# Performance work log

Measured on AMD Instinct MI355X. Metric: run time of the kernel, lower is better.

## Reference

```python
import jax, jax.numpy as jnp
import numpy as np
from jax import lax

B, D, T = 8, 128, 4096
Q, C = 30, 1024


def setup_inputs() -> dict:
    key = jax.random.key(0)
    k1, k2 = jax.random.split(key)
    x = jax.random.normal(k1, (B, D, T), dtype=jnp.float32)
    codebooks = jax.random.normal(k2, (Q, C, D), dtype=jnp.float32)
    return {"x": x, "codebooks": codebooks}


def _vq_step(residual, cb):
    # residual: [B, T, D], cb: [C, D]
    # argmin over squared euclidean distance; ||r||^2 term is constant per row
    scores = -2.0 * jnp.einsum("btd,cd->btc", residual, cb) + jnp.sum(cb * cb, axis=-1)  # [B,T,C]
    idx = jnp.argmin(scores, axis=-1)          # [B,T]
    quant = cb[idx]                            # [B,T,D] gather
    # commitment loss: mse(quantize.detach(), residual)
    loss = jnp.mean((lax.stop_gradient(quant) - residual) ** 2)
    # straight-through estimator
    quant_st = residual + lax.stop_gradient(quant - residual)
    new_residual = residual - lax.stop_gradient(quant)
    return new_residual, (quant_st, loss)


def reference(x, codebooks):
    # x: [B, D, T] -> [B, T, D]
    xt = jnp.transpose(x, (0, 2, 1))
    _, (quants, losses) = lax.scan(_vq_step, xt, codebooks)  # quants: [Q,B,T,D]
    quantized = jnp.sum(quants, axis=0)                      # [B,T,D]
    quantized = jnp.transpose(quantized, (0, 2, 1))          # [B,D,T]
    commit_loss = jnp.sum(losses)
    return quantized, commit_loss
```

## Files before the change

### kernel.cpp

```cpp
#include <hip/hip_runtime.h>
#include <stdint.h>

#define B_ 8
#define D_ 128
#define T_ 4096
#define Q_ 30
#define C_ 1024

typedef __attribute__((ext_vector_type(8))) _Float16 half8;
typedef __attribute__((ext_vector_type(4))) float float4_;

__device__ __align__(16) _Float16 g_half[(size_t)Q_*8*16384];

typedef __attribute__((address_space(3))) void lds_void;
typedef __attribute__((address_space(1))) const void gbl_void;
__device__ __forceinline__ void gld16(const void* g, void* l){
  __builtin_amdgcn_global_load_lds((gbl_void*)g, (lds_void*)l, 16, 0, 0);
}

__global__ void rvq_prep(const float* __restrict__ cb, float* __restrict__ sumsq){
  int g    = blockIdx.x*128 + (threadIdx.x>>1);
  int half = threadIdx.x & 1;
  const float* src = cb + (size_t)g*D_ + half*64;
  double s = 0.0;
#pragma unroll
  for (int i=0;i<64;i+=4){
    float4_ f = *(const float4_*)(src+i);
    s += (double)f.x*f.x + (double)f.y*f.y + (double)f.z*f.z + (double)f.w*f.w;
  }
  s += __shfl_xor(s, 1);
  if (!half) sumsq[g] = (float)s;
}

__global__ void rvq_split(const float* __restrict__ cb){
  const int bI   = blockIdx.x;
  const int tid  = threadIdx.x;
  const int crel = tid>>1, part = tid&1;
  const int swz  = crel & 15;
  const float* src = cb + ((size_t)bI*128 + crel)*128 + part*64;
  _Float16* dst = g_half + ((size_t)bI<<14) + (crel<<7);
#pragma unroll
  for (int i=0;i<8;++i){
    float4_ f0 = *(const float4_*)(src + i*8);
    float4_ f1 = *(const float4_*)(src + i*8 + 4);
    half8 h;
    h[0]=(_Float16)f0.x; h[1]=(_Float16)f0.y; h[2]=(_Float16)f0.z; h[3]=(_Float16)f0.w;
    h[4]=(_Float16)f1.x; h[5]=(_Float16)f1.y; h[6]=(_Float16)f1.z; h[7]=(_Float16)f1.w;
    const int kg  = part*8 + i;
    const int kgs = kg ^ swz;
    *(half8*)&dst[kgs<<3] = h;
  }
}

__global__ __launch_bounds__(256,1) void rvq_main(
    const float* __restrict__ x, const float* __restrict__ cb,
    const float* __restrict__ sumsq, double* __restrict__ lossAcc,
    float* __restrict__ out)
{
  __shared__ _Float16 sBh[2*16384];
  __shared__ float sCS[4][32][16][2];
  __shared__ int   sCI[4][32][16][2];
  __shared__ int   sI4[4][32][4];
  __shared__ float sCcQ[1024];

  const int tid  = threadIdx.x;
  const int wv   = tid>>6;
  const int ln   = tid&63;
  const int col  = ln&15;
  const int quad = ln>>4;
  const int blk  = blockIdx.x;
  const int b    = blk>>5;
  const int t0   = ((blk&31)<<7) + (wv<<5);

  double rmast[2][4][8];
#pragma unroll
  for (int rt=0;rt<2;++rt){
    const int t = t0 + rt*16 + col;
#pragma unroll
    for (int kc=0;kc<4;++kc)
#pragma unroll
      for (int j=0;j<8;++j){
        const int d = kc*32 + quad*8 + j;
        rmast[rt][kc][j] = (double)x[((size_t)b*D_ + d)*T_ + t];
      }
  }

  half8 ah[2][4];
  auto makeAB = [&](){
#pragma unroll
    for (int rt=0;rt<2;++rt)
#pragma unroll
      for (int kc=0;kc<4;++kc){
        half8 h;
#pragma unroll
        for (int j=0;j<8;++j) h[j] = (_Float16)(float)rmast[rt][kc][j];
        ah[rt][kc] = h;
      }
  };
  makeAB();

  auto stage = [&](int c){
    const char* gsrc = (const char*)g_half + ((size_t)c<<15) + (wv<<13) + (ln<<4);
    char* ldst = (char*)sBh + ((c&1)<<15) + (wv<<13) + (ln<<4);
#pragma unroll
    for (int it=0; it<8; ++it)
      gld16(gsrc + it*1024, ldst + it*1024);
  };

  for (int i=tid; i<1024; i+=256) sCcQ[i] = sumsq[i];
  stage(0);
  __syncthreads();

  double lossd = 0.0;

  for (int q=0;q<Q_;++q){
    const float* cbq = cb + (size_t)q*C_*D_;

    float m1[2][4], m2[2][4]; int i1[2][4], i2[2][4];
#pragma unroll
    for (int rt=0;rt<2;++rt)
#pragma unroll
      for (int rg=0;rg<4;++rg){
        m1[rt][rg]=3.0e38f; i1[rt][rg]=0;
        m2[rt][rg]=3.0e38f; i2[rt][rg]=0;
      }

    for (int ch=0; ch<8; ++ch){
      const int gstep = q*8 + ch;
      const int nxt   = (gstep+1 < Q_*8) ? gstep+1 : 0;
      stage(nxt);
      asm volatile("s_waitcnt vmcnt(8)" ::: "memory");
      asm volatile("s_barrier" ::: "memory");
      const int slot = (gstep&1)<<14;

#pragma unroll
      for (int itc=0; itc<4; ++itc){
        float4_ acc[2][2];
#pragma unroll
        for (int a=0;a<2;++a)
#pragma unroll
          for (int c2=0;c2<2;++c2) acc[a][c2] = (float4_){0.f,0.f,0.f,0.f};
#pragma unroll
        for (int kc=0;kc<4;++kc){
          const int kgs = ((kc<<2) + quad) ^ col;
          half8 bf[2];
#pragma unroll
          for (int ct=0;ct<2;++ct){
            const int n = itc*32 + ct*16 + col;
            bf[ct] = *(const half8*)&sBh[slot + (n<<7) + (kgs<<3)];
          }
#pragma unroll
          for (int rt=0;rt<2;++rt)
#pragma unroll
            for (int ct=0;ct<2;++ct)
              acc[rt][ct] = __builtin_amdgcn_mfma_f32_16x16x32_f16(ah[rt][kc], bf[ct], acc[rt][ct], 0,0,0);
        }
#pragma unroll
        for (int ct=0;ct<2;++ct){
          const float cc = sCcQ[(ch<<7) + itc*32 + ct*16 + col];
          const int cid  = ch*8 + itc*2 + ct;
#pragma unroll
          for (int rt=0;rt<2;++rt)
#pragma unroll
            for (int rg=0;rg<4;++rg){
              float s = fmaf(-2.0f, acc[rt][ct][rg], cc);
              if (s < m1[rt][rg]) {
                m2[rt][rg]=m1[rt][rg]; i2[rt][rg]=i1[rt][rg];
                m1[rt][rg]=s;          i1[rt][rg]=cid;
              } else if (s < m2[rt][rg]) {
                m2[rt][rg]=s;          i2[rt][rg]=cid;
              }
            }
        }
      }
      if (ch != 7)
        asm volatile("s_barrier" ::: "memory");
    }

#pragma unroll
    for (int rt=0;rt<2;++rt)
#pragma unroll
      for (int rg=0;rg<4;++rg){
        const int row = rt*16 + quad*4 + rg;
        sCS[wv][row][col][0] = m1[rt][rg];  sCI[wv][row][col][0] = (i1[rt][rg]<<4)+col;
        sCS[wv][row][col][1] = m2[rt][rg];  sCI[wv][row][col][1] = (i2[rt][rg]<<4)+col;
      }

    if (ln < 32){
      const int row = ln;
      float b0=3.0e38f,b1=3.0e38f,b2=3.0e38f,b3=3.0e38f;
      int   e0=0x7fffffff,e1=0x7fffffff,e2=0x7fffffff,e3=0x7fffffff;
#pragma unroll
      for (int c2=0;c2<32;++c2){
        const float s = sCS[wv][row][c2>>1][c2&1];
        const int  id = sCI[wv][row][c2>>1][c2&1];
        const bool l0 = (s<b0)||(s==b0&&id<e0);
        const bool l1 = (s<b1)||(s==b1&&id<e1);
        const bool l2 = (s<b2)||(s==b2&&id<e2);
        const bool l3 = (s<b3)||(s==b3&&id<e3);
        if (l3){
          b3 = l2 ? b2 : s;  e3 = l2 ? e2 : id;
          if (l2){
            b2 = l1 ? b1 : s;  e2 = l1 ? e1 : id;
            if (l1){
              b1 = l0 ? b0 : s;  e1 = l0 ? e0 : id;
              if (l0){ b0 = s; e0 = id; }
            }
          }
        }
      }
      sI4[wv][row][0]=e0; sI4[wv][row][1]=e1; sI4[wv][row][2]=e2; sI4[wv][row][3]=e3;
    }

#pragma unroll
    for (int rt=0;rt<2;++rt){
      const int m = rt*16 + col;
      double bestS = 1.0e300; int bestJ = 0x7fffffff;
#pragma unroll
      for (int cnd=0;cnd<4;++cnd){
        const int jj = sI4[wv][m][cnd];
        const float* p = cbq + ((size_t)jj<<7) + (quad<<3);
        double s = 0.0;
#pragma unroll
        for (int kc=0;kc<4;++kc){
          float4_ a0 = *(const float4_*)(p + kc*32);
          float4_ a1 = *(const float4_*)(p + kc*32 + 4);
          float fv[8] = {a0.x,a0.y,a0.z,a0.w,a1.x,a1.y,a1.z,a1.w};
#pragma unroll
          for (int j=0;j<8;++j){
            double cd = (double)fv[j];
            s += cd*(cd - 2.0*rmast[rt][kc][j]);
          }
        }
        s += __shfl_xor(s, 16); s += __shfl_xor(s, 32);
        if ((s < bestS) || (s == bestS && jj < bestJ)){ bestS = s; bestJ = jj; }
      }
      const float* pw = cbq + ((size_t)bestJ<<7) + (quad<<3);
#pragma unroll
      for (int kc=0;kc<4;++kc){
        float4_ w0 = *(const float4_*)(pw + kc*32);
        float4_ w1 = *(const float4_*)(pw + kc*32 + 4);
        float fw[8] = {w0.x,w0.y,w0.z,w0.w,w1.x,w1.y,w1.z,w1.w};
#pragma unroll
        for (int j=0;j<8;++j){
          double rn = rmast[rt][kc][j] - (double)fw[j];
          rmast[rt][kc][j] = rn;
          lossd += rn*rn;
        }
      }
    }
    makeAB();
    if (q+1 < Q_){
      for (int i=tid; i<1024; i+=256) sCcQ[i] = sumsq[(q+1)*1024 + i];
    }
    __syncthreads();
  }

#pragma unroll
  for (int rt=0;rt<2;++rt){
    const int t = t0 + rt*16 + col;
#pragma unroll
    for (int kc=0;kc<4;++kc)
#pragma unroll
      for (int j=0;j<8;++j){
        const int d = kc*32 + quad*8 + j;
        const size_t o = ((size_t)b*D_ + d)*T_ + t;
        out[o] = (float)((double)x[o] - rmast[rt][kc][j]);
      }
  }
#pragma unroll
  for (int mk=1; mk<64; mk<<=1) lossd += __shfl_xor(lossd, mk);
  if (ln==0) atomicAdd(lossAcc, lossd);
}

__global__ void rvq_fin(const double* __restrict__ lossAcc, float* __restrict__ out){
  out[(size_t)B_*D_*T_] = (float)(*lossAcc * (1.0/((double)B_*(double)D_*(double)T_)));
}

extern "C" void kernel_launch(void* const* d_in, const int* in_sizes, int n_in,
                              void* d_out, int out_size, void* d_ws, size_t ws_size,
                              hipStream_t stream) {
  const float* x  = (const float*)d_in[0];
  const float* cb = (const float*)d_in[1];
  float* out      = (float*)d_out;
  double* lossAcc = (double*)d_ws;
  float*  sumsq   = (float*)((char*)d_ws + 256);

  hipMemsetAsync(d_ws, 0, 256, stream);
  rvq_prep <<<Q_*C_/128, 256, 0, stream>>>(cb, sumsq);
  rvq_split<<<Q_*8,      256, 0, stream>>>(cb);
  rvq_main <<<(B_*T_)/128, 256, 0, stream>>>(x, cb, sumsq, lossAcc, out);
  rvq_fin  <<<1, 1, 0, stream>>>(lossAcc, out);
}
```

Baseline: 1.944 ms.

## Give each wave a private triple-buffered LDS ring to drop workgroup barriers

```diff
diff --git a/kernel.cpp b/kernel.cpp
--- a/kernel.cpp
+++ b/kernel.cpp
@@ -10,7 +10,7 @@
 typedef __attribute__((ext_vector_type(8))) _Float16 half8;
 typedef __attribute__((ext_vector_type(4))) float float4_;
 
-__device__ __align__(16) _Float16 g_half[(size_t)Q_*8*16384];
+__device__ __align__(16) _Float16 g_half[(size_t)Q_*32*4096];
 
 typedef __attribute__((address_space(3))) void lds_void;
 typedef __attribute__((address_space(1))) const void gbl_void;
@@ -33,20 +33,21 @@
 }
 
 __global__ void rvq_split(const float* __restrict__ cb){
-  const int bI   = blockIdx.x;
+  const int gs   = blockIdx.x;
   const int tid  = threadIdx.x;
-  const int crel = tid>>1, part = tid&1;
+  const int crel = tid>>3;
+  const int part = tid&7;
   const int swz  = crel & 15;
-  const float* src = cb + ((size_t)bI*128 + crel)*128 + part*64;
-  _Float16* dst = g_half + ((size_t)bI<<14) + (crel<<7);
-#pragma unroll
-  for (int i=0;i<8;++i){
+  const float* src = cb + ((size_t)gs*32 + crel)*128 + part*16;
+  _Float16* dst = g_half + ((size_t)gs<<12) + (crel<<7);
+#pragma unroll
+  for (int i=0;i<2;++i){
     float4_ f0 = *(const float4_*)(src + i*8);
     float4_ f1 = *(const float4_*)(src + i*8 + 4);
     half8 h;
     h[0]=(_Float16)f0.x; h[1]=(_Float16)f0.y; h[2]=(_Float16)f0.z; h[3]=(_Float16)f0.w;
     h[4]=(_Float16)f1.x; h[5]=(_Float16)f1.y; h[6]=(_Float16)f1.z; h[7]=(_Float16)f1.w;
-    const int kg  = part*8 + i;
+    const int kg  = part*2 + i;
     const int kgs = kg ^ swz;
     *(half8*)&dst[kgs<<3] = h;
   }
@@ -57,9 +58,9 @@
     const float* __restrict__ sumsq, double* __restrict__ lossAcc,
     float* __restrict__ out)
 {
-  __shared__ _Float16 sBh[2*16384];
-  __shared__ float sCS[4][32][16][2];
-  __shared__ int   sCI[4][32][16][2];
+  __shared__ _Float16 sRing[4][3][4096];
+  __shared__ float sCS[4][32][34];
+  __shared__ int   sCI[4][32][34];
   __shared__ int   sI4[4][32][4];
   __shared__ float sCcQ[1024];
 
@@ -99,16 +100,16 @@
   };
   makeAB();
 
-  auto stage = [&](int c){
-    const char* gsrc = (const char*)g_half + ((size_t)c<<15) + (wv<<13) + (ln<<4);
-    char* ldst = (char*)sBh + ((c&1)<<15) + (wv<<13) + (ln<<4);
+  auto stage = [&](int gs){
+    const char* gsrc = (const char*)g_half + ((size_t)gs<<13) + (ln<<4);
+    char* ldst = (char*)&sRing[wv][gs%3][0] + (ln<<4);
 #pragma unroll
     for (int it=0; it<8; ++it)
       gld16(gsrc + it*1024, ldst + it*1024);
   };
 
   for (int i=tid; i<1024; i+=256) sCcQ[i] = sumsq[i];
-  stage(0);
+  stage(0); stage(1);
   __syncthreads();
 
   double lossd = 0.0;
@@ -125,56 +126,53 @@
         m2[rt][rg]=3.0e38f; i2[rt][rg]=0;
       }
 
-    for (int ch=0; ch<8; ++ch){
-      const int gstep = q*8 + ch;
-      const int nxt   = (gstep+1 < Q_*8) ? gstep+1 : 0;
-      stage(nxt);
-      asm volatile("s_waitcnt vmcnt(8)" ::: "memory");
-      asm volatile("s_barrier" ::: "memory");
-      const int slot = (gstep&1)<<14;
-
-#pragma unroll
-      for (int itc=0; itc<4; ++itc){
-        float4_ acc[2][2];
-#pragma unroll
-        for (int a=0;a<2;++a)
-#pragma unroll
-          for (int c2=0;c2<2;++c2) acc[a][c2] = (float4_){0.f,0.f,0.f,0.f};
-#pragma unroll
-        for (int kc=0;kc<4;++kc){
-          const int kgs = ((kc<<2) + quad) ^ col;
-          half8 bf[2];
-#pragma unroll
-          for (int ct=0;ct<2;++ct){
-            const int n = itc*32 + ct*16 + col;
-            bf[ct] = *(const half8*)&sBh[slot + (n<<7) + (kgs<<3)];
+    for (int s=0; s<32; ++s){
+      const int gs = q*32 + s;
+      if (gs+2 < Q_*32){
+        stage(gs+2);
+        asm volatile("s_waitcnt vmcnt(16)" ::: "memory");
+      } else {
+        asm volatile("s_waitcnt vmcnt(0)" ::: "memory");
+      }
+      const _Float16* base = &sRing[wv][gs%3][0];
+
+      float4_ acc[2][2];
+#pragma unroll
+      for (int a=0;a<2;++a)
+#pragma unroll
+        for (int c2=0;c2<2;++c2) acc[a][c2] = (float4_){0.f,0.f,0.f,0.f};
+#pragma unroll
+      for (int kc=0;kc<4;++kc){
+        const int kgs = ((kc<<2) + quad) ^ col;
+        half8 bf[2];
+#pragma unroll
+        for (int ct=0;ct<2;++ct){
+          const int n = ct*16 + col;
+          bf[ct] = *(const half8*)&base[(n<<7) + (kgs<<3)];
+        }
+#pragma unroll
+        for (int rt=0;rt<2;++rt)
+#pragma unroll
+          for (int ct=0;ct<2;++ct)
+            acc[rt][ct] = __builtin_amdgcn_mfma_f32_16x16x32_f16(ah[rt][kc], bf[ct], acc[rt][ct], 0,0,0);
+      }
+#pragma unroll
+      for (int ct=0;ct<2;++ct){
+        const int cid = s*2 + ct;
+        const float cc = sCcQ[(cid<<4) + col];
+#pragma unroll
+        for (int rt=0;rt<2;++rt)
+#pragma unroll
+          for (int rg=0;rg<4;++rg){
+            float sc = fmaf(-2.0f, acc[rt][ct][rg], cc);
+            if (sc < m1[rt][rg]) {
+              m2[rt][rg]=m1[rt][rg]; i2[rt][rg]=i1[rt][rg];
+              m1[rt][rg]=sc;         i1[rt][rg]=cid;
+            } else if (sc < m2[rt][rg]) {
+              m2[rt][rg]=sc;         i2[rt][rg]=cid;
+            }
           }
-#pragma unroll
-          for (int rt=0;rt<2;++rt)
-#pragma unroll
-            for (int ct=0;ct<2;++ct)
-              acc[rt][ct] = __builtin_amdgcn_mfma_f32_16x16x32_f16(ah[rt][kc], bf[ct], acc[rt][ct], 0,0,0);
-        }
-#pragma unroll
-        for (int ct=0;ct<2;++ct){
-          const float cc = sCcQ[(ch<<7) + itc*32 + ct*16 + col];
-          const int cid  = ch*8 + itc*2 + ct;
-#pragma unroll
-          for (int rt=0;rt<2;++rt)
-#pragma unroll
-            for (int rg=0;rg<4;++rg){
-              float s = fmaf(-2.0f, acc[rt][ct][rg], cc);
-              if (s < m1[rt][rg]) {
-                m2[rt][rg]=m1[rt][rg]; i2[rt][rg]=i1[rt][rg];
-                m1[rt][rg]=s;          i1[rt][rg]=cid;
-              } else if (s < m2[rt][rg]) {
-                m2[rt][rg]=s;          i2[rt][rg]=cid;
-              }
-            }
-        }
-      }
-      if (ch != 7)
-        asm volatile("s_barrier" ::: "memory");
+      }
     }
 
 #pragma unroll
@@ -182,8 +180,8 @@
 #pragma unroll
       for (int rg=0;rg<4;++rg){
         const int row = rt*16 + quad*4 + rg;
-        sCS[wv][row][col][0] = m1[rt][rg];  sCI[wv][row][col][0] = (i1[rt][rg]<<4)+col;
-        sCS[wv][row][col][1] = m2[rt][rg];  sCI[wv][row][col][1] = (i2[rt][rg]<<4)+col;
+        sCS[wv][row][col*2+0] = m1[rt][rg];  sCI[wv][row][col*2+0] = (i1[rt][rg]<<4)+col;
+        sCS[wv][row][col*2+1] = m2[rt][rg];  sCI[wv][row][col*2+1] = (i2[rt][rg]<<4)+col;
       }
 
     if (ln < 32){
@@ -192,19 +190,19 @@
       int   e0=0x7fffffff,e1=0x7fffffff,e2=0x7fffffff,e3=0x7fffffff;
 #pragma unroll
       for (int c2=0;c2<32;++c2){
-        const float s = sCS[wv][row][c2>>1][c2&1];
-        const int  id = sCI[wv][row][c2>>1][c2&1];
-        const bool l0 = (s<b0)||(s==b0&&id<e0);
-        const bool l1 = (s<b1)||(s==b1&&id<e1);
-        const bool l2 = (s<b2)||(s==b2&&id<e2);
-        const bool l3 = (s<b3)||(s==b3&&id<e3);
+        const float sc = sCS[wv][row][c2];
+        const int  id  = sCI[wv][row][c2];
+        const bool l0 = (sc<b0)||(sc==b0&&id<e0);
+        const bool l1 = (sc<b1)||(sc==b1&&id<e1);
+        const bool l2 = (sc<b2)||(sc==b2&&id<e2);
+        const bool l3 = (sc<b3)||(sc==b3&&id<e3);
         if (l3){
-          b3 = l2 ? b2 : s;  e3 = l2 ? e2 : id;
+          b3 = l2 ? b2 : sc;  e3 = l2 ? e2 : id;
           if (l2){
-            b2 = l1 ? b1 : s;  e2 = l1 ? e1 : id;
+            b2 = l1 ? b1 : sc;  e2 = l1 ? e1 : id;
             if (l1){
-              b1 = l0 ? b0 : s;  e1 = l0 ? e0 : id;
-              if (l0){ b0 = s; e0 = id; }
+              b1 = l0 ? b0 : sc;  e1 = l0 ? e0 : id;
+              if (l0){ b0 = sc; e0 = id; }
             }
           }
         }
@@ -220,7 +218,7 @@
       for (int cnd=0;cnd<4;++cnd){
         const int jj = sI4[wv][m][cnd];
         const float* p = cbq + ((size_t)jj<<7) + (quad<<3);
-        double s = 0.0;
+        double sd = 0.0;
 #pragma unroll
         for (int kc=0;kc<4;++kc){
           float4_ a0 = *(const float4_*)(p + kc*32);
@@ -229,11 +227,11 @@
 #pragma unroll
           for (int j=0;j<8;++j){
             double cd = (double)fv[j];
-            s += cd*(cd - 2.0*rmast[rt][kc][j]);
+            sd += cd*(cd - 2.0*rmast[rt][kc][j]);
           }
         }
-        s += __shfl_xor(s, 16); s += __shfl_xor(s, 32);
-        if ((s < bestS) || (s == bestS && jj < bestJ)){ bestS = s; bestJ = jj; }
+        sd += __shfl_xor(sd, 16); sd += __shfl_xor(sd, 32);
+        if ((sd < bestS) || (sd == bestS && jj < bestJ)){ bestS = sd; bestJ = jj; }
       }
       const float* pw = cbq + ((size_t)bestJ<<7) + (quad<<3);
 #pragma unroll
@@ -252,8 +250,8 @@
     makeAB();
     if (q+1 < Q_){
       for (int i=tid; i<1024; i+=256) sCcQ[i] = sumsq[(q+1)*1024 + i];
-    }
-    __syncthreads();
+      __syncthreads();
+    }
   }
 
 #pragma unroll
@@ -288,7 +286,7 @@
 
   hipMemsetAsync(d_ws, 0, 256, stream);
   rvq_prep <<<Q_*C_/128, 256, 0, stream>>>(cb, sumsq);
-  rvq_split<<<Q_*8,      256, 0, stream>>>(cb);
+  rvq_split<<<Q_*32,     256, 0, stream>>>(cb);
   rvq_main <<<(B_*T_)/128, 256, 0, stream>>>(x, cb, sumsq, lossAcc, out);
   rvq_fin  <<<1, 1, 0, stream>>>(lossAcc, out);
 }
```

Measured after the change: 2.197 ms. 13.0% more time.
